# Optimization experiments

Measured on AMD Instinct MI355X. Metric: run time of the kernel, lower is better.

Reference implementation:

```python
import jax, jax.numpy as jnp
import numpy as np

N = 100000      # nodes
E = 3200000     # edges (avg degree 32)
F_IN = 512
HID = 256
CLS = 64


def _linear_init(k, fan_in, fan_out):
    lim = 1.0 / np.sqrt(fan_in)
    kw, kb = jax.random.split(k)
    W = jax.random.uniform(kw, (fan_in, fan_out), jnp.float32, -lim, lim)
    b = jax.random.uniform(kb, (fan_out,), jnp.float32, -lim, lim)
    return W, b


def setup_inputs() -> dict:
    key = jax.random.key(0)
    ks = jax.random.split(key, 8)
    x = jax.random.normal(ks[0], (N, F_IN), jnp.float32)
    edge_src = jax.random.randint(ks[1], (E,), 0, N, jnp.int32)
    off = jax.random.randint(ks[2], (E,), 1, N, jnp.int32)
    edge_dst = ((edge_src + off) % N).astype(jnp.int32)  # no self loops
    Wm0, bm0 = _linear_init(ks[3], F_IN, HID)
    Wv0, bv0 = _linear_init(ks[4], F_IN, HID)
    Wm1, bm1 = _linear_init(ks[5], HID, CLS)
    Wv1, bv1 = _linear_init(ks[6], HID, CLS)
    sample = jax.random.normal(ks[7], (N, CLS), jnp.float32)
    return dict(x=x, Wm0=Wm0, bm0=bm0, Wv0=Wv0, bv0=bv0,
                Wm1=Wm1, bm1=bm1, Wv1=Wv1, bv1=bv1,
                sample=sample, edge_src=edge_src, edge_dst=edge_dst)


def reference(x, Wm0, bm0, Wv0, bv0, Wm1, bm1, Wv1, bv1, sample, edge_src, edge_dst):
    n = x.shape[0]
    loops = jnp.arange(n, dtype=edge_src.dtype)
    src = jnp.concatenate([edge_src, loops])  # fill_diag(adj, 1.0)
    dst = jnp.concatenate([edge_dst, loops])
    ones = jnp.ones(src.shape[0], x.dtype)
    deg = jax.ops.segment_sum(ones, src, num_segments=n)
    dis = jnp.where(deg > 0, deg ** -0.5, 0.0)   # D^-0.5
    di = jnp.where(deg > 0, 1.0 / deg, 0.0)      # D^-1
    w0 = dis[src] * dis[dst]                      # adj0 = D^-0.5 A D^-0.5
    w1 = di[src] * di[dst]                        # adj1 = D^-1  A D^-1

    def spmm(w, m):  # (adj @ m) with edge weights w
        return jax.ops.segment_sum(w[:, None] * m[dst], src, num_segments=n)

    # layer 0 (initial=True): no aggregation, dropout off (eval)
    mean = jax.nn.elu(x @ Wm0 + bm0)
    var = jax.nn.relu(x @ Wv0 + bv0)
    # layer 1: variance-attention + dual SpMM
    mean = jax.nn.elu(mean @ Wm1 + bm1)
    var = jax.nn.relu(var @ Wv1 + bv1) + 1e-6
    attn = jnp.exp(-var)
    mean = spmm(w0, mean * attn)
    var = spmm(w1, var * attn * attn)

    out = mean + sample * jnp.sqrt(var)
    return jax.nn.log_softmax(out, axis=-1)
```

## Files before the change

kernel.cpp:

```cpp
#include <hip/hip_runtime.h>
#include <cstdint>
#include <cstddef>


typedef _Float16 h8 __attribute__((ext_vector_type(8)));
typedef _Float16 h2 __attribute__((ext_vector_type(2)));
typedef float f32x4 __attribute__((ext_vector_type(4)));
typedef unsigned int uint32;

#define BSHIFT 7
#define NCHUNK 256

static __device__ __forceinline__ float elu_f(float z) {
  return z > 0.f ? z : expm1f(z);
}

__global__ __launch_bounds__(256) void hist_k(const int* __restrict__ esrc, int E,
                                              int chunk, int* __restrict__ h, int NB) {
  __shared__ int sh[1024];
  int t = threadIdx.x;
  for (int i = t; i < NB; i += 256) sh[i] = 0;
  __syncthreads();
  int e0 = blockIdx.x * chunk;
  int e1 = min(e0 + chunk, E);
  for (int e = e0 + t; e < e1; e += 256) atomicAdd(&sh[esrc[e] >> BSHIFT], 1);
  __syncthreads();
  for (int i = t; i < NB; i += 256) h[blockIdx.x * NB + i] = sh[i];
}

__global__ __launch_bounds__(256) void btotal_k(const int* __restrict__ h,
                                                int* __restrict__ tot, int NB) {
  int b = blockIdx.x, t = threadIdx.x;
  int v = h[t * NB + b];
#pragma unroll
  for (int off = 32; off; off >>= 1) v += __shfl_xor(v, off, 64);
  __shared__ int sw[4];
  if ((t & 63) == 0) sw[t >> 6] = v;
  __syncthreads();
  if (t == 0) tot[b] = sw[0] + sw[1] + sw[2] + sw[3];
}

__global__ __launch_bounds__(1024) void bscan_k(const int* __restrict__ tot,
                                                int* __restrict__ base, int NB) {
  __shared__ int sh[1024];
  int t = threadIdx.x;
  int v = (t < NB) ? tot[t] : 0;
  sh[t] = v;
  __syncthreads();
  for (int off = 1; off < 1024; off <<= 1) {
    int add = (t >= off) ? sh[t - off] : 0;
    __syncthreads();
    sh[t] += add;
    __syncthreads();
  }
  if (t < NB) base[t] = sh[t] - v;
  if (t == 1023) base[NB] = sh[1023];
}

__global__ __launch_bounds__(256) void boff_k(int* __restrict__ h,
                                              const int* __restrict__ base, int NB) {
  __shared__ int sh[256];
  int b = blockIdx.x, t = threadIdx.x;
  int v = h[t * NB + b];
  sh[t] = v;
  __syncthreads();
  for (int off = 1; off < 256; off <<= 1) {
    int add = (t >= off) ? sh[t - off] : 0;
    __syncthreads();
    sh[t] += add;
    __syncthreads();
  }
  h[t * NB + b] = base[b] + sh[t] - v;
}

__global__ __launch_bounds__(256) void bscatter_k(
    const int* __restrict__ esrc, const int* __restrict__ edst, int E, int chunk,
    const int* __restrict__ h, int2* __restrict__ pairs, int NB) {
  __shared__ int lcur[1024];
  int t = threadIdx.x;
  for (int i = t; i < NB; i += 256) lcur[i] = h[blockIdx.x * NB + i];
  __syncthreads();
  int e0 = blockIdx.x * chunk;
  int e1 = min(e0 + chunk, E);
  for (int e = e0 + t; e < e1; e += 256) {
    int s = esrc[e], d = edst[e];
    int pos = atomicAdd(&lcur[s >> BSHIFT], 1);
    pairs[pos] = make_int2(s, d);
  }
}

__global__ __launch_bounds__(256) void countN_k(
    const int2* __restrict__ pairs, const int* __restrict__ base,
    int* __restrict__ cnt, float2* __restrict__ dd, int n) {
  __shared__ int c128[128];
  int b = blockIdx.x, t = threadIdx.x;
  if (t < 128) c128[t] = 0;
  __syncthreads();
  int lo = base[b], hi = base[b + 1];
  for (int i = lo + t; i < hi; i += 256) atomicAdd(&c128[pairs[i].x & 127], 1);
  __syncthreads();
  if (t < 128) {
    int node = b * 128 + t;
    if (node < n) {
      int c = c128[t];
      cnt[node] = c;
      float d = (float)(c + 1);
      dd[node] = make_float2(rsqrtf(d), 1.f / d);
    }
  }
}

__global__ __launch_bounds__(256) void partC_k(
    const int2* __restrict__ pairs, const int* __restrict__ base,
    const int* __restrict__ rs, int* __restrict__ csr, int n) {
  __shared__ int lcur[128];
  int b = blockIdx.x, t = threadIdx.x;
  if (t < 128) {
    int node = b * 128 + t;
    lcur[t] = (node < n) ? rs[node] : 0;
  }
  __syncthreads();
  int lo = base[b], hi = base[b + 1];
  for (int i = lo + t; i < hi; i += 256) {
    int2 pr = pairs[i];
    int pos = atomicAdd(&lcur[pr.x & 127], 1);
    csr[pos] = pr.y;
  }
}

__global__ void scan1_k(const int* __restrict__ cnt, int* __restrict__ excl,
                        int* __restrict__ bsum, int n) {
  __shared__ int sh[256];
  int t = threadIdx.x, idx = blockIdx.x * 256 + t;
  int v = (idx < n) ? ((cnt[idx] + 3) & ~3) : 0;
  sh[t] = v;
  __syncthreads();
  for (int off = 1; off < 256; off <<= 1) {
    int add = (t >= off) ? sh[t - off] : 0;
    __syncthreads();
    sh[t] += add;
    __syncthreads();
  }
  if (idx < n) excl[idx] = sh[t] - v;
  if (t == 255) bsum[blockIdx.x] = sh[255];
}

__global__ void scan2_k(const int* __restrict__ bsum, int* __restrict__ boff, int nb) {
  __shared__ int sh[512];
  int t = threadIdx.x;
  int v = (t < nb) ? bsum[t] : 0;
  sh[t] = v;
  __syncthreads();
  for (int off = 1; off < 512; off <<= 1) {
    int add = (t >= off) ? sh[t - off] : 0;
    __syncthreads();
    sh[t] += add;
    __syncthreads();
  }
  if (t < nb) boff[t] = sh[t] - v;
}

__global__ void scan3_k(int* __restrict__ excl, const int* __restrict__ boff, int n) {
  int idx = blockIdx.x * 256 + threadIdx.x;
  if (idx < n) excl[idx] += boff[blockIdx.x];
}

__global__ void prep_w_k(const float* __restrict__ Wm0, const float* __restrict__ Wv0,
                         const float* __restrict__ Wm1, const float* __restrict__ Wv1,
                         _Float16* __restrict__ W1t, _Float16* __restrict__ W2t) {
  int idx = blockIdx.x * 256 + threadIdx.x;
  if (idx < 512 * 512) {
    int n = idx >> 9, k = idx & 511;
    float v = (n < 256) ? Wm0[k * 256 + n] : Wv0[k * 256 + (n - 256)];
    W1t[idx] = (_Float16)v;
  }
  if (idx < 128 * 512) {
    int n = idx >> 9, k = idx & 511;
    float v = 0.f;
    if (n < 64) { if (k < 256) v = Wm1[k * 64 + n]; }
    else        { if (k >= 256) v = Wv1[(k - 256) * 64 + (n - 64)]; }
    W2t[idx] = (_Float16)v;
  }
}

__global__ __launch_bounds__(256) void gemm1_k(
    const float* __restrict__ A, const _Float16* __restrict__ Bt,
    const float* __restrict__ b0, const float* __restrict__ b1,
    _Float16* __restrict__ out, int M, int K, int mtiles) {
  __shared__ _Float16 lds[20480];
  _Float16* As = lds;
  _Float16* Bs = lds + 10240;

  const int sg = blockIdx.x >> 5, loc = blockIdx.x & 31;
  const int nt = loc >> 3, mtl = loc & 7;
  const int mt = sg * 8 + mtl;
  if (mt >= mtiles) return;
  const int m0 = mt * 128, n0 = nt * 128;
  const int t = threadIdx.x;
  const int lane = t & 63;
  const int wave = t >> 6;
  const int wm = wave >> 1, wn = wave & 1;
  const int lr = lane & 15, quad = lane >> 4;
  const int trow = t >> 2;
  const int tkc = (t & 3) * 8;

  const size_t arow0 = (size_t)min(m0 + trow, M - 1) * K;
  const size_t arow1 = (size_t)min(m0 + trow + 64, M - 1) * K;
  const size_t brow0 = (size_t)(n0 + trow) * K;
  const size_t brow1 = (size_t)(n0 + trow + 64) * K;

  f32x4 acc[4][4] = {};
  float4 pa[2][2];
  h8 pb[2];

  {
    const float* s0 = A + arow0 + tkc;
    const float* s1 = A + arow1 + tkc;
    pa[0][0] = ((const float4*)s0)[0]; pa[0][1] = ((const float4*)s0)[1];
    pa[1][0] = ((const float4*)s1)[0]; pa[1][1] = ((const float4*)s1)[1];
    pb[0] = *(const h8*)(Bt + brow0 + tkc);
    pb[1] = *(const h8*)(Bt + brow1 + tkc);
  }
  {
    *(h8*)&As[trow * 40 + tkc] =
        h8{(_Float16)pa[0][0].x, (_Float16)pa[0][0].y, (_Float16)pa[0][0].z, (_Float16)pa[0][0].w,
           (_Float16)pa[0][1].x, (_Float16)pa[0][1].y, (_Float16)pa[0][1].z, (_Float16)pa[0][1].w};
    *(h8*)&As[(trow + 64) * 40 + tkc] =
        h8{(_Float16)pa[1][0].x, (_Float16)pa[1][0].y, (_Float16)pa[1][0].z, (_Float16)pa[1][0].w,
           (_Float16)pa[1][1].x, (_Float16)pa[1][1].y, (_Float16)pa[1][1].z, (_Float16)pa[1][1].w};
    *(h8*)&Bs[trow * 40 + tkc] = pb[0];
    *(h8*)&Bs[(trow + 64) * 40 + tkc] = pb[1];
  }
  __syncthreads();

  for (int kt = 0; kt < K; kt += 32) {
    const int cur = (kt >> 5) & 1;
    const int curo = cur * 5120;
    const bool more = (kt + 32) < K;
    if (more) {
      const float* s0 = A + arow0 + kt + 32 + tkc;
      const float* s1 = A + arow1 + kt + 32 + tkc;
      pa[0][0] = ((const float4*)s0)[0]; pa[0][1] = ((const float4*)s0)[1];
      pa[1][0] = ((const float4*)s1)[0]; pa[1][1] = ((const float4*)s1)[1];
      pb[0] = *(const h8*)(Bt + brow0 + kt + 32 + tkc);
      pb[1] = *(const h8*)(Bt + brow1 + kt + 32 + tkc);
    }
    h8 af[4], bf[4];
#pragma unroll
    for (int i = 0; i < 4; i++)
      af[i] = *(h8*)&As[curo + (wm * 64 + i * 16 + lr) * 40 + quad * 8];
#pragma unroll
    for (int j = 0; j < 4; j++)
      bf[j] = *(h8*)&Bs[curo + (wn * 64 + j * 16 + lr) * 40 + quad * 8];
#pragma unroll
    for (int i = 0; i < 4; i++)
#pragma unroll
      for (int j = 0; j < 4; j++)
        acc[i][j] = __builtin_amdgcn_mfma_f32_16x16x32_f16(af[i], bf[j], acc[i][j], 0, 0, 0);
    if (more) {
      const int nxto = (cur ^ 1) * 5120;
      *(h8*)&As[nxto + trow * 40 + tkc] =
          h8{(_Float16)pa[0][0].x, (_Float16)pa[0][0].y, (_Float16)pa[0][0].z, (_Float16)pa[0][0].w,
             (_Float16)pa[0][1].x, (_Float16)pa[0][1].y, (_Float16)pa[0][1].z, (_Float16)pa[0][1].w};
      *(h8*)&As[nxto + (trow + 64) * 40 + tkc] =
          h8{(_Float16)pa[1][0].x, (_Float16)pa[1][0].y, (_Float16)pa[1][0].z, (_Float16)pa[1][0].w,
             (_Float16)pa[1][1].x, (_Float16)pa[1][1].y, (_Float16)pa[1][1].z, (_Float16)pa[1][1].w};
      *(h8*)&Bs[nxto + trow * 40 + tkc] = pb[0];
      *(h8*)&Bs[nxto + (trow + 64) * 40 + tkc] = pb[1];
      __syncthreads();
    }
  }

  __syncthreads();
#pragma unroll
  for (int j = 0; j < 4; j++) {
    int gc = n0 + wn * 64 + j * 16 + lr;
    float bj = (gc < 256) ? b0[gc] : b1[gc - 256];
#pragma unroll
    for (int i = 0; i < 4; i++) {
#pragma unroll
      for (int r = 0; r < 4; r++) {
        float z = acc[i][j][r] + bj;
        float v = (gc < 256) ? elu_f(z) : fmaxf(z, 0.f);
        lds[(wm * 64 + i * 16 + quad * 4 + r) * 136 + wn * 64 + j * 16 + lr] = (_Float16)v;
      }
    }
  }
  __syncthreads();
  {
    const int row = t >> 1, col0 = (t & 1) * 64;
    const int gr = m0 + row;
    if (gr < M) {
      _Float16* dst = out + (size_t)gr * 512 + n0 + col0;
#pragma unroll
      for (int k = 0; k < 8; k++)
        *(h8*)(dst + k * 8) = *(h8*)&lds[row * 136 + col0 + k * 8];
    }
  }
}

__global__ __launch_bounds__(256) void gemm2_k(
    const _Float16* __restrict__ A, const _Float16* __restrict__ Bt,
    const float* __restrict__ bm1, const float* __restrict__ bv1,
    uint32* __restrict__ Mcat, int M, int K) {
  __shared__ _Float16 lds[20480];
  _Float16* As = lds;
  _Float16* Bs = lds + 10240;
  const int m0 = blockIdx.x * 128;
  const int t = threadIdx.x;
  const int lane = t & 63;
  const int wave = t >> 6;
  const int lr = lane & 15, quad = lane >> 4;
  const int trow = t >> 2;
  const int tkc = (t & 3) * 8;

  const size_t arow0 = (size_t)min(m0 + trow, M - 1) * K;
  const size_t arow1 = (size_t)min(m0 + trow + 64, M - 1) * K;
  const size_t brow0 = (size_t)trow * K;
  const size_t brow1 = (size_t)(trow + 64) * K;

  f32x4 acc[2][8] = {};
  h8 pa[2], pb[2];

  pa[0] = *(const h8*)(A + arow0 + tkc);
  pa[1] = *(const h8*)(A + arow1 + tkc);
  pb[0] = *(const h8*)(Bt + brow0 + tkc);
  pb[1] = *(const h8*)(Bt + brow1 + tkc);
  *(h8*)&As[trow * 40 + tkc] = pa[0];
  *(h8*)&As[(trow + 64) * 40 + tkc] = pa[1];
  *(h8*)&Bs[trow * 40 + tkc] = pb[0];
  *(h8*)&Bs[(trow + 64) * 40 + tkc] = pb[1];
  __syncthreads();

  for (int kt = 0; kt < K; kt += 32) {
    const int cur = (kt >> 5) & 1;
    const int curo = cur * 5120;
    const bool more = (kt + 32) < K;
    if (more) {
      pa[0] = *(const h8*)(A + arow0 + kt + 32 + tkc);
      pa[1] = *(const h8*)(A + arow1 + kt + 32 + tkc);
      pb[0] = *(const h8*)(Bt + brow0 + kt + 32 + tkc);
      pb[1] = *(const h8*)(Bt + brow1 + kt + 32 + tkc);
    }
    h8 af[2], bf[8];
#pragma unroll
    for (int i = 0; i < 2; i++)
      af[i] = *(h8*)&As[curo + (wave * 32 + i * 16 + lr) * 40 + quad * 8];
#pragma unroll
    for (int j = 0; j < 8; j++)
      bf[j] = *(h8*)&Bs[curo + (j * 16 + lr) * 40 + quad * 8];
#pragma unroll
    for (int i = 0; i < 2; i++)
#pragma unroll
      for (int j = 0; j < 8; j++)
        acc[i][j] = __builtin_amdgcn_mfma_f32_16x16x32_f16(af[i], bf[j], acc[i][j], 0, 0, 0);
    if (more) {
      const int nxto = (cur ^ 1) * 5120;
      *(h8*)&As[nxto + trow * 40 + tkc] = pa[0];
      *(h8*)&As[nxto + (trow + 64) * 40 + tkc] = pa[1];
      *(h8*)&Bs[nxto + trow * 40 + tkc] = pb[0];
      *(h8*)&Bs[nxto + (trow + 64) * 40 + tkc] = pb[1];
      __syncthreads();
    }
  }

#pragma unroll
  for (int jm = 0; jm < 4; jm++) {
    int c = jm * 16 + lr;
    float bm = bm1[c], bv = bv1[c];
#pragma unroll
    for (int i = 0; i < 2; i++) {
#pragma unroll
      for (int r = 0; r < 4; r++) {
        int gr = m0 + wave * 32 + i * 16 + quad * 4 + r;
        if (gr < M) {
          float zm = acc[i][jm][r] + bm;
          float zv = acc[i][4 + jm][r] + bv;
          float m = elu_f(zm);
          float v = fmaxf(zv, 0.f) + 1e-6f;
          float a = __expf(-v);
          h2 pk;
          pk.x = (_Float16)(m * a);
          pk.y = (_Float16)(v * a * a);
          Mcat[(size_t)gr * 64 + c] = __builtin_bit_cast(uint32, pk);
        }
      }
    }
  }
}

__global__ __launch_bounds__(256) void spmm_final_k(
    const uint32* __restrict__ Mcat, const float2* __restrict__ dd,
    const int* __restrict__ row_start, const int* __restrict__ cnt,
    const int* __restrict__ csr, const float* __restrict__ sample,
    float* __restrict__ out, int n) {
  int wid = threadIdx.x >> 6, lane = threadIdx.x & 63;
  int r = blockIdx.x * 4 + wid;
  if (r >= n) return;
  float2 wr = dd[r];
  h2 self = __builtin_bit_cast(h2, Mcat[(size_t)r * 64 + lane]);
  float Sm = wr.x * (float)self.x;
  float Sv = wr.y * (float)self.y;
  int start = __builtin_amdgcn_readfirstlane(row_start[r]);
  int c = __builtin_amdgcn_readfirstlane(cnt[r]);
  int j = 0;
  for (; j + 4 <= c; j += 4) {
    int4 d4 = *(const int4*)(csr + start + j);
    float2 w0 = dd[d4.x];
    float2 w1 = dd[d4.y];
    float2 w2 = dd[d4.z];
    float2 w3 = dd[d4.w];
    h2 p0 = __builtin_bit_cast(h2, Mcat[(size_t)d4.x * 64 + lane]);
    h2 p1 = __builtin_bit_cast(h2, Mcat[(size_t)d4.y * 64 + lane]);
    h2 p2 = __builtin_bit_cast(h2, Mcat[(size_t)d4.z * 64 + lane]);
    h2 p3 = __builtin_bit_cast(h2, Mcat[(size_t)d4.w * 64 + lane]);
    Sm += w0.x * (float)p0.x; Sv += w0.y * (float)p0.y;
    Sm += w1.x * (float)p1.x; Sv += w1.y * (float)p1.y;
    Sm += w2.x * (float)p2.x; Sv += w2.y * (float)p2.y;
    Sm += w3.x * (float)p3.x; Sv += w3.y * (float)p3.y;
  }
  for (; j < c; j++) {
    int d = csr[start + j];
    float2 w = dd[d];
    h2 p = __builtin_bit_cast(h2, Mcat[(size_t)d * 64 + lane]);
    Sm += w.x * (float)p.x;
    Sv += w.y * (float)p.y;
  }
  float mean = wr.x * Sm;
  float var = wr.y * Sv;
  float o = mean + sample[(size_t)r * 64 + lane] * sqrtf(var);
  float mx = o;
#pragma unroll
  for (int off = 32; off; off >>= 1) mx = fmaxf(mx, __shfl_xor(mx, off, 64));
  float ex = __expf(o - mx);
  float s = ex;
#pragma unroll
  for (int off = 32; off; off >>= 1) s += __shfl_xor(s, off, 64);
  out[(size_t)r * 64 + lane] = o - mx - logf(s);
}

extern "C" void kernel_launch(void* const* d_in, const int* in_sizes, int n_in,
                              void* d_out, int out_size, void* d_ws, size_t ws_size,
                              hipStream_t stream) {
  (void)n_in; (void)out_size; (void)ws_size;
  const float* x    = (const float*)d_in[0];
  const float* Wm0  = (const float*)d_in[1];
  const float* bm0  = (const float*)d_in[2];
  const float* Wv0  = (const float*)d_in[3];
  const float* bv0  = (const float*)d_in[4];
  const float* Wm1  = (const float*)d_in[5];
  const float* bm1  = (const float*)d_in[6];
  const float* Wv1  = (const float*)d_in[7];
  const float* bv1  = (const float*)d_in[8];
  const float* sample = (const float*)d_in[9];
  const int* esrc   = (const int*)d_in[10];
  const int* edst   = (const int*)d_in[11];
  float* out = (float*)d_out;

  const int N = in_sizes[0] / 512;
  const int E = in_sizes[10];
  const int NB = (N + 127) >> BSHIFT;
  const int chunk = (E + NCHUNK - 1) / NCHUNK;

  uint8_t* p = (uint8_t*)d_ws;
  size_t off = 0;
  auto alloc = [&](size_t bytes) -> void* {
    void* r = p + off;
    off += (bytes + 255) & ~(size_t)255;
    return r;
  };
  _Float16* W1t  = (_Float16*)alloc((size_t)512 * 512 * 2);
  _Float16* W2t  = (_Float16*)alloc((size_t)128 * 512 * 2);
  _Float16* Hcat = (_Float16*)alloc((size_t)N * 512 * 2);
  uint32*   Mcat = (uint32*)alloc((size_t)N * 64 * 4);
  int*   cnt    = (int*)alloc((size_t)N * 4);
  float2* dd    = (float2*)alloc((size_t)N * 8);
  int*   rs     = (int*)alloc((size_t)N * 4);
  int*   h      = (int*)alloc((size_t)NCHUNK * NB * 4);
  int*   tot    = (int*)alloc((size_t)(NB + 1) * 4);
  int*   base   = (int*)alloc((size_t)(NB + 1) * 4);
  int*   bsum   = (int*)alloc(2048);
  int*   boff   = (int*)alloc(2048);
  int*   csr    = (int*)alloc((size_t)(E + 4 * N) * 4);
  int2* pairs = (int2*)Hcat;

  const int nbN = (N + 255) / 256;

  prep_w_k<<<(512 * 512 + 255) / 256, 256, 0, stream>>>(Wm0, Wv0, Wm1, Wv1, W1t, W2t);
  hist_k<<<NCHUNK, 256, 0, stream>>>(esrc, E, chunk, h, NB);
  btotal_k<<<NB, 256, 0, stream>>>(h, tot, NB);
  bscan_k<<<1, 1024, 0, stream>>>(tot, base, NB);
  boff_k<<<NB, 256, 0, stream>>>(h, base, NB);
  bscatter_k<<<NCHUNK, 256, 0, stream>>>(esrc, edst, E, chunk, h, pairs, NB);
  countN_k<<<NB, 256, 0, stream>>>(pairs, base, cnt, dd, N);
  scan1_k<<<nbN, 256, 0, stream>>>(cnt, rs, bsum, N);
  scan2_k<<<1, 512, 0, stream>>>(bsum, boff, nbN);
  scan3_k<<<nbN, 256, 0, stream>>>(rs, boff, N);
  partC_k<<<NB, 256, 0, stream>>>(pairs, base, rs, csr, N);

  const int mtiles = (N + 127) / 128;
  const int sgroups = (mtiles + 7) / 8;
  gemm1_k<<<sgroups * 32, 256, 0, stream>>>(x, W1t, bm0, bv0, Hcat, N, 512, mtiles);
  gemm2_k<<<mtiles, 256, 0, stream>>>(Hcat, W2t, bm1, bv1, Mcat, N, 512);
  spmm_final_k<<<(N + 3) / 4, 256, 0, stream>>>(Mcat, dd, rs, cnt, csr, sample, out, N);
}
```

Measured before the change: 759.8 us.

## Rewrite gemm1 with full-width N tiles and direct global-to-LDS loads

gemm1 now gives each 512-thread block a 128-row tile across the full 512 output columns, instead of four separate 128x128 tiles that each reread the same fp32 rows of x. Tiles are staged with global_load_lds straight into XOR-swizzled, double-buffered LDS, and the fp32-to-fp16 conversion moves to fragment-read time. The goal is to cut redundant global traffic on the large fp32 input and the register round-trip through VGPRs. In exchange it uses 96KB of LDS per block and a large accumulator array, which limits occupancy, and it converts A to fp16 once per wave that reads it rather than once per tile.

```diff
diff --git a/kernel.cpp b/kernel.cpp
--- a/kernel.cpp
+++ b/kernel.cpp
@@ -13,6 +13,12 @@
 
 static __device__ __forceinline__ float elu_f(float z) {
   return z > 0.f ? z : expm1f(z);
+}
+
+static __device__ __forceinline__ void gload16(const void* g, void* l) {
+  __builtin_amdgcn_global_load_lds(
+      (__attribute__((address_space(1))) void*)g,
+      (__attribute__((address_space(3))) void*)l, 16, 0, 0);
 }
 
 __global__ __launch_bounds__(256) void hist_k(const int* __restrict__ esrc, int E,
@@ -183,119 +189,108 @@
   }
 }
 
-__global__ __launch_bounds__(256) void gemm1_k(
+__global__ __launch_bounds__(512, 2) void gemm1_k(
     const float* __restrict__ A, const _Float16* __restrict__ Bt,
     const float* __restrict__ b0, const float* __restrict__ b1,
-    _Float16* __restrict__ out, int M, int K, int mtiles) {
-  __shared__ _Float16 lds[20480];
-  _Float16* As = lds;
-  _Float16* Bs = lds + 10240;
-
-  const int sg = blockIdx.x >> 5, loc = blockIdx.x & 31;
-  const int nt = loc >> 3, mtl = loc & 7;
-  const int mt = sg * 8 + mtl;
-  if (mt >= mtiles) return;
-  const int m0 = mt * 128, n0 = nt * 128;
+    _Float16* __restrict__ out, int M) {
+  __shared__ __align__(16) unsigned char ldsb[98304];
+
+  const int m0 = blockIdx.x * 128;
   const int t = threadIdx.x;
   const int lane = t & 63;
   const int wave = t >> 6;
-  const int wm = wave >> 1, wn = wave & 1;
+  const int wm = wave >> 2;
+  const int wn = wave & 3;
   const int lr = lane & 15, quad = lane >> 4;
-  const int trow = t >> 2;
-  const int tkc = (t & 3) * 8;
-
-  const size_t arow0 = (size_t)min(m0 + trow, M - 1) * K;
-  const size_t arow1 = (size_t)min(m0 + trow + 64, M - 1) * K;
-  const size_t brow0 = (size_t)(n0 + trow) * K;
-  const size_t brow1 = (size_t)(n0 + trow + 64) * K;
-
-  f32x4 acc[4][4] = {};
-  float4 pa[2][2];
-  h8 pb[2];
-
-  {
-    const float* s0 = A + arow0 + tkc;
-    const float* s1 = A + arow1 + tkc;
-    pa[0][0] = ((const float4*)s0)[0]; pa[0][1] = ((const float4*)s0)[1];
-    pa[1][0] = ((const float4*)s1)[0]; pa[1][1] = ((const float4*)s1)[1];
-    pb[0] = *(const h8*)(Bt + brow0 + tkc);
-    pb[1] = *(const h8*)(Bt + brow1 + tkc);
-  }
-  {
-    *(h8*)&As[trow * 40 + tkc] =
-        h8{(_Float16)pa[0][0].x, (_Float16)pa[0][0].y, (_Float16)pa[0][0].z, (_Float16)pa[0][0].w,
-           (_Float16)pa[0][1].x, (_Float16)pa[0][1].y, (_Float16)pa[0][1].z, (_Float16)pa[0][1].w};
-    *(h8*)&As[(trow + 64) * 40 + tkc] =
-        h8{(_Float16)pa[1][0].x, (_Float16)pa[1][0].y, (_Float16)pa[1][0].z, (_Float16)pa[1][0].w,
-           (_Float16)pa[1][1].x, (_Float16)pa[1][1].y, (_Float16)pa[1][1].z, (_Float16)pa[1][1].w};
-    *(h8*)&Bs[trow * 40 + tkc] = pb[0];
-    *(h8*)&Bs[(trow + 64) * 40 + tkc] = pb[1];
-  }
-  __syncthreads();
-
-  for (int kt = 0; kt < K; kt += 32) {
-    const int cur = (kt >> 5) & 1;
-    const int curo = cur * 5120;
-    const bool more = (kt + 32) < K;
-    if (more) {
-      const float* s0 = A + arow0 + kt + 32 + tkc;
-      const float* s1 = A + arow1 + kt + 32 + tkc;
-      pa[0][0] = ((const float4*)s0)[0]; pa[0][1] = ((const float4*)s0)[1];
-      pa[1][0] = ((const float4*)s1)[0]; pa[1][1] = ((const float4*)s1)[1];
-      pb[0] = *(const h8*)(Bt + brow0 + kt + 32 + tkc);
-      pb[1] = *(const h8*)(Bt + brow1 + kt + 32 + tkc);
-    }
-    h8 af[4], bf[4];
-#pragma unroll
-    for (int i = 0; i < 4; i++)
-      af[i] = *(h8*)&As[curo + (wm * 64 + i * 16 + lr) * 40 + quad * 8];
-#pragma unroll
-    for (int j = 0; j < 4; j++)
-      bf[j] = *(h8*)&Bs[curo + (wn * 64 + j * 16 + lr) * 40 + quad * 8];
-#pragma unroll
-    for (int i = 0; i < 4; i++)
-#pragma unroll
-      for (int j = 0; j < 4; j++)
-        acc[i][j] = __builtin_amdgcn_mfma_f32_16x16x32_f16(af[i], bf[j], acc[i][j], 0, 0, 0);
-    if (more) {
-      const int nxto = (cur ^ 1) * 5120;
-      *(h8*)&As[nxto + trow * 40 + tkc] =
-          h8{(_Float16)pa[0][0].x, (_Float16)pa[0][0].y, (_Float16)pa[0][0].z, (_Float16)pa[0][0].w,
-             (_Float16)pa[0][1].x, (_Float16)pa[0][1].y, (_Float16)pa[0][1].z, (_Float16)pa[0][1].w};
-      *(h8*)&As[nxto + (trow + 64) * 40 + tkc] =
-          h8{(_Float16)pa[1][0].x, (_Float16)pa[1][0].y, (_Float16)pa[1][0].z, (_Float16)pa[1][0].w,
-             (_Float16)pa[1][1].x, (_Float16)pa[1][1].y, (_Float16)pa[1][1].z, (_Float16)pa[1][1].w};
-      *(h8*)&Bs[nxto + trow * 40 + tkc] = pb[0];
-      *(h8*)&Bs[nxto + (trow + 64) * 40 + tkc] = pb[1];
-      __syncthreads();
-    }
-  }
-
-  __syncthreads();
-#pragma unroll
-  for (int j = 0; j < 4; j++) {
-    int gc = n0 + wn * 64 + j * 16 + lr;
-    float bj = (gc < 256) ? b0[gc] : b1[gc - 256];
+
+  const int ra = t >> 3;
+  const int sa = t & 7;
+  const int asw = (sa ^ (ra & 7)) << 2;
+  const int rb = t >> 2;
+  const int sb = t & 3;
+  const int bsw = (sb ^ (rb & 3)) << 3;
+
+  f32x4 acc[4][8] = {};
+
+  auto stage = [&](int b, int kt) {
+#pragma unroll
+    for (int i = 0; i < 2; i++) {
+      int r = i * 64 + ra;
+      const float* src = A + (size_t)min(m0 + r, M - 1) * 512 + kt + asw;
+      gload16(src, ldsb + b * 16384 + i * 8192 + t * 16);
+    }
 #pragma unroll
     for (int i = 0; i < 4; i++) {
-#pragma unroll
-      for (int r = 0; r < 4; r++) {
-        float z = acc[i][j][r] + bj;
-        float v = (gc < 256) ? elu_f(z) : fmaxf(z, 0.f);
-        lds[(wm * 64 + i * 16 + quad * 4 + r) * 136 + wn * 64 + j * 16 + lr] = (_Float16)v;
+      int r = i * 128 + rb;
+      const _Float16* src = Bt + (size_t)r * 512 + kt + bsw;
+      gload16(src, ldsb + 32768 + b * 32768 + i * 8192 + t * 16);
+    }
+  };
+
+  stage(0, 0);
+  __syncthreads();
+
+  int cur = 0;
+  const int zA = lr & 7;
+  const int zB = lr & 3;
+  for (int kt = 0; kt < 512; kt += 32) {
+    if (kt + 32 < 512) stage(cur ^ 1, kt + 32);
+    const unsigned char* Ab = ldsb + cur * 16384;
+    const unsigned char* Bb = ldsb + 32768 + cur * 32768;
+    h8 bf[8];
+#pragma unroll
+    for (int j = 0; j < 8; j++) {
+      int row = wn * 128 + j * 16 + lr;
+      bf[j] = *(const h8*)(Bb + row * 64 + ((quad ^ zB) << 4));
+    }
+#pragma unroll
+    for (int i = 0; i < 4; i++) {
+      int R = wm * 64 + i * 16 + lr;
+      const float4 a0 = *(const float4*)(Ab + R * 128 + (((2 * quad) ^ zA) << 4));
+      const float4 a1 = *(const float4*)(Ab + R * 128 + (((2 * quad + 1) ^ zA) << 4));
+      h8 af = {(_Float16)a0.x, (_Float16)a0.y, (_Float16)a0.z, (_Float16)a0.w,
+               (_Float16)a1.x, (_Float16)a1.y, (_Float16)a1.z, (_Float16)a1.w};
+#pragma unroll
+      for (int j = 0; j < 8; j++)
+        acc[i][j] = __builtin_amdgcn_mfma_f32_16x16x32_f16(af, bf[j], acc[i][j], 0, 0, 0);
+    }
+    __syncthreads();
+    cur ^= 1;
+  }
+
+  _Float16* lt = (_Float16*)ldsb;
+  for (int hh = 0; hh < 2; hh++) {
+    if (wm == hh) {
+#pragma unroll
+      for (int j = 0; j < 8; j++) {
+        int col = wn * 128 + j * 16 + lr;
+        float bj = (col < 256) ? b0[col] : b1[col - 256];
+#pragma unroll
+        for (int i = 0; i < 4; i++) {
+#pragma unroll
+          for (int r = 0; r < 4; r++) {
+            float z = acc[i][j][r] + bj;
+            float v = (col < 256) ? elu_f(z) : fmaxf(z, 0.f);
+            lt[(i * 16 + quad * 4 + r) * 520 + col] = (_Float16)v;
+          }
+        }
       }
     }
-  }
-  __syncthreads();
-  {
-    const int row = t >> 1, col0 = (t & 1) * 64;
-    const int gr = m0 + row;
-    if (gr < M) {
-      _Float16* dst = out + (size_t)gr * 512 + n0 + col0;
-#pragma unroll
-      for (int k = 0; k < 8; k++)
-        *(h8*)(dst + k * 8) = *(h8*)&lds[row * 136 + col0 + k * 8];
-    }
+    __syncthreads();
+    {
+      int row = t >> 3;
+      int gr = m0 + hh * 64 + row;
+      if (gr < M) {
+        _Float16* dst = out + (size_t)gr * 512;
+        const _Float16* srow = lt + row * 520;
+#pragma unroll
+        for (int k = 0; k < 8; k++) {
+          int c0 = ((t & 7) + k * 8) * 8;
+          *(h8*)(dst + c0) = *(const h8*)(srow + c0);
+        }
+      }
+    }
+    __syncthreads();
   }
 }
 
@@ -499,8 +494,7 @@
   partC_k<<<NB, 256, 0, stream>>>(pairs, base, rs, csr, N);
 
   const int mtiles = (N + 127) / 128;
-  const int sgroups = (mtiles + 7) / 8;
-  gemm1_k<<<sgroups * 32, 256, 0, stream>>>(x, W1t, bm0, bv0, Hcat, N, 512, mtiles);
+  gemm1_k<<<mtiles, 512, 0, stream>>>(x, W1t, bm0, bv0, Hcat, N);
   gemm2_k<<<mtiles, 256, 0, stream>>>(Hcat, W2t, bm1, bv1, Mcat, N, 512);
   spmm_final_k<<<(N + 3) / 4, 256, 0, stream>>>(Mcat, dd, rs, cnt, csr, sample, out, N);
 }
```

Result: slower. 796.8 us (+4.9%).
